# Kernel tuning notes

Measured on AMD Instinct MI355X. Metric: run time of the kernel, lower is better.

## Reference

```python
import jax, jax.numpy as jnp
import numpy as np

EPS = 1e-5

def layer_norm(x, g, b):
    mu = jnp.mean(x, axis=-1, keepdims=True)
    var = jnp.mean(jnp.square(x - mu), axis=-1, keepdims=True)
    return (x - mu) * jax.lax.rsqrt(var + EPS) * g + b

def setup_inputs() -> dict:
    key = jax.random.key(0)
    B, N, IN_D, S, D = 64, 4096, 256, 8, 256
    ks = jax.random.split(key, 20)
    scale = lambda fan_in: 1.0 / np.sqrt(fan_in)
    u = lambda k, shape, s: jax.random.uniform(k, shape, jnp.float32, -s, s)
    return {
        "inputs": jax.random.normal(ks[0], (B, N, IN_D), jnp.float32),
        "noise": jax.random.normal(ks[1], (B, S, D), jnp.float32),
        "slots_mu": jax.random.normal(ks[2], (1, S, D), jnp.float32),
        "slots_sigma": jnp.ones((1, S, D), jnp.float32) * 0.1,
        "Wq": u(ks[3], (D, D), scale(D)), "bq": u(ks[4], (D,), scale(D)),
        "Wk": u(ks[5], (D, IN_D), scale(IN_D)), "bk": u(ks[6], (D,), scale(IN_D)),
        "Wv": u(ks[7], (D, IN_D), scale(IN_D)), "bv": u(ks[8], (D,), scale(IN_D)),
        "W_ih": u(ks[9], (3 * D, D), scale(D)), "b_ih": u(ks[10], (3 * D,), scale(D)),
        "W_hh": u(ks[11], (3 * D, D), scale(D)), "b_hh": u(ks[12], (3 * D,), scale(D)),
        "W1": u(ks[13], (D, D), scale(D)), "b1": u(ks[14], (D,), scale(D)),
        "W2": u(ks[15], (D, D), scale(D)), "b2": u(ks[16], (D,), scale(D)),
        "ln_slots_g": jnp.ones((D,), jnp.float32), "ln_slots_b": jnp.zeros((D,), jnp.float32),
        "ln_mlp_g": jnp.ones((D,), jnp.float32), "ln_mlp_b": jnp.zeros((D,), jnp.float32),
    }

def gru_cell(x, h, W_ih, b_ih, W_hh, b_hh):
    # PyTorch GRUCell: gates ordered (reset, update, new)
    gi = x @ W_ih.T + b_ih  # [B*S, 3D]
    gh = h @ W_hh.T + b_hh
    i_r, i_z, i_n = jnp.split(gi, 3, axis=-1)
    h_r, h_z, h_n = jnp.split(gh, 3, axis=-1)
    r = jax.nn.sigmoid(i_r + h_r)
    z = jax.nn.sigmoid(i_z + h_z)
    n = jnp.tanh(i_n + r * h_n)
    return (1.0 - z) * n + z * h

def reference(inputs, noise, slots_mu, slots_sigma, Wq, bq, Wk, bk, Wv, bv,
              W_ih, b_ih, W_hh, b_hh, W1, b1, W2, b2,
              ln_slots_g, ln_slots_b, ln_mlp_g, ln_mlp_b):
    B, N, _ = inputs.shape
    _, S, D = noise.shape
    num_iterations = 3
    slots = slots_mu + slots_sigma * noise  # [B, S, D]
    # k, v are loop-invariant; hoist the big GEMMs out of the iteration loop
    k = jnp.einsum('bnd,ed->bne', inputs, Wk) + bk  # [B, N, D]
    v = jnp.einsum('bnd,ed->bne', inputs, Wv) + bv  # [B, N, D]
    inv_sqrt_d = 1.0 / np.sqrt(D)
    for _ in range(num_iterations):
        slots_prev = slots
        q = layer_norm(slots, ln_slots_g, ln_slots_b) @ Wq.T + bq  # [B, S, D]
        attn_logits = jnp.einsum('bsd,bnd->bsn', q, k) * inv_sqrt_d
        attn = jax.nn.softmax(attn_logits, axis=-1)  # softmax over inputs (dim=-1)
        updates = jnp.einsum('bsn,bnd->bsd', attn, v)  # [B, S, D]
        h_new = gru_cell(updates.reshape(-1, D), slots_prev.reshape(-1, D),
                         W_ih, b_ih, W_hh, b_hh).reshape(B, S, D)
        slots = slots_prev + h_new  # residual around GRU (as in source)
        hidden = jax.nn.relu(layer_norm(slots, ln_mlp_g, ln_mlp_b) @ W1.T + b1)
        slots = slots + (hidden @ W2.T + b2)
    return slots
```

## Files before the change

kernel.cpp:

```cpp
#include <hip/hip_runtime.h>


constexpr int Bn = 64;
constexpr int Nn = 4096;
constexpr int Dd = 256;
constexpr int Ss = 8;
constexpr int CH = 16;
constexpr float EPSF = 1e-5f;

#define DEV __device__ __forceinline__

using short8 = __attribute__((ext_vector_type(8))) short;
using f32x4 = __attribute__((ext_vector_type(4))) float;
union U8 { short8 s; uint4 u; };

DEV unsigned bfpack2(float lo, float hi) {
  unsigned ul = __float_as_uint(lo), uh = __float_as_uint(hi);
  ul = (ul + 0x7FFFu + ((ul >> 16) & 1u)) >> 16;
  uh = (uh + 0x7FFFu + ((uh >> 16) & 1u)) & 0xFFFF0000u;
  return ul | uh;
}
DEV unsigned short bf16r(float x) {
  unsigned u = __float_as_uint(x);
  u = (u + 0x7FFFu + ((u >> 16) & 1u)) >> 16;
  return (unsigned short)u;
}
DEV float rsum32(float v) {
  v += __shfl_xor(v, 1); v += __shfl_xor(v, 2); v += __shfl_xor(v, 4);
  v += __shfl_xor(v, 8); v += __shfl_xor(v, 16);
  return v;
}
DEV float sigm(float x) { return 1.f / (1.f + __expf(-x)); }

template <int NK>
DEV void load_af(short8* a, const unsigned short* base, int lda, int m16, int quad) {
  const unsigned short* p = base + m16 * lda + quad * 8;
#pragma unroll
  for (int kk = 0; kk < NK; ++kk) a[kk] = *(const short8*)(p + kk * 32);
}
template <int NK>
DEV f32x4 gemm_tile(const short8* a, const unsigned short* wr, float binit) {
  f32x4 acc = {binit, binit, binit, binit};
#pragma unroll
  for (int kk = 0; kk < NK; ++kk) {
    short8 b = *(const short8*)(wr + kk * 32);
    acc = __builtin_amdgcn_mfma_f32_16x16x32_bf16(a[kk], b, acc, 0, 0, 0);
  }
  return acc;
}

DEV void ln_row8(const float* x, const float* g, const float* b, int d0,
                 unsigned short* dst) {
  float s = x[0] + x[1] + x[2] + x[3] + x[4] + x[5] + x[6] + x[7];
  float mu = rsum32(s) * (1.f / 256.f);
  float q = 0.f;
#pragma unroll
  for (int j = 0; j < 8; ++j) { float d = x[j] - mu; q += d * d; }
  float rs = rsqrtf(rsum32(q) * (1.f / 256.f) + EPSF);
  float o[8];
#pragma unroll
  for (int j = 0; j < 8; ++j) o[j] = (x[j] - mu) * rs * g[d0 + j] + b[d0 + j];
  uint4 w;
  w.x = bfpack2(o[0], o[1]); w.y = bfpack2(o[2], o[3]);
  w.z = bfpack2(o[4], o[5]); w.w = bfpack2(o[6], o[7]);
  *(uint4*)dst = w;
}

__global__ __launch_bounds__(256) void k_wqk(const float* __restrict__ Wq,
                                             const float* __restrict__ Wk,
                                             const float* __restrict__ bq,
                                             unsigned short* __restrict__ Wqk_b,
                                             float* __restrict__ bqk) {
  int tid = threadIdx.x, c = blockIdx.x;
  if (c < 256) {
    float acc = 0.f;
    for (int e = 0; e < 256; ++e) acc += Wq[e * 256 + tid] * Wk[e * 256 + c];
    Wqk_b[c * 256 + tid] = bf16r(acc);
  } else {
    float acc = 0.f;
    for (int e = 0; e < 256; ++e) acc += bq[e] * Wk[e * 256 + tid];
    bqk[tid] = acc;
  }
}

__global__ __launch_bounds__(256) void k_conv(
    const float* __restrict__ Wv, const float* __restrict__ Wih,
    const float* __restrict__ Whh, const float* __restrict__ W1,
    const float* __restrict__ W2,
    const float* __restrict__ bih, const float* __restrict__ bhh,
    unsigned* Wv_b, unsigned* Wzr_b, unsigned* Win_b, unsigned* Whn_b,
    unsigned* W1_b, unsigned* W2_b, float* bzr) {
  if (blockIdx.x >= 1152) {
    int i = (blockIdx.x - 1152) * 256 + threadIdx.x;
    if (i < 512) bzr[i] = bih[i] + bhh[i];
    return;
  }
  int p = blockIdx.x * 256 + threadIdx.x;
  const float* src; unsigned* dst;
  if (p < 32768) { src = Wv + 2 * p; dst = Wv_b + p; }
  else if (p < 163840) {
    int q = p - 32768, row = q >> 8, col = (q & 255) * 2;
    src = (col < 256) ? (Wih + row * 256 + col) : (Whh + row * 256 + col - 256);
    dst = Wzr_b + q;
  }
  else if (p < 196608) { int q = p - 163840; src = Wih + 512 * 256 + 2 * q; dst = Win_b + q; }
  else if (p < 229376) { int q = p - 196608; src = Whh + 512 * 256 + 2 * q; dst = Whn_b + q; }
  else if (p < 262144) { int q = p - 229376; src = W1 + 2 * q; dst = W1_b + q; }
  else { int q = p - 262144; src = W2 + 2 * q; dst = W2_b + q; }
  dst[0] = bfpack2(src[0], src[1]);
}

__global__ __launch_bounds__(512) void k_qk0(const float* __restrict__ noise,
                                             const float* __restrict__ s_mu,
                                             const float* __restrict__ s_sg,
                                             const float* __restrict__ gsl,
                                             const float* __restrict__ bsl,
                                             const unsigned short* __restrict__ Wqk_b,
                                             const float* __restrict__ bqk,
                                             float* __restrict__ slots,
                                             float* __restrict__ qk) {
  __shared__ __align__(16) unsigned short lnb[16 * 264];
  const int tid = threadIdx.x, bb = blockIdx.x;
  const int lane = tid & 63, wave = tid >> 6;
  const int m16 = lane & 15, quad = lane >> 4;
  const int row = tid >> 5, l32 = tid & 31, d0 = l32 * 8;
  {
    const int grow = bb * 16 + row;
    const int sidx = (grow & 7) * 256 + d0;
    const float* np = noise + (size_t)grow * 256 + d0;
    float4 n0 = *(const float4*)np, n1 = *(const float4*)(np + 4);
    float4 m0 = *(const float4*)(s_mu + sidx), m1 = *(const float4*)(s_mu + sidx + 4);
    float4 g0 = *(const float4*)(s_sg + sidx), g1 = *(const float4*)(s_sg + sidx + 4);
    float x[8] = {m0.x + g0.x * n0.x, m0.y + g0.y * n0.y,
                  m0.z + g0.z * n0.z, m0.w + g0.w * n0.w,
                  m1.x + g1.x * n1.x, m1.y + g1.y * n1.y,
                  m1.z + g1.z * n1.z, m1.w + g1.w * n1.w};
    float* sp_ = slots + (size_t)grow * 256 + d0;
    float4 o0, o1;
    o0.x = x[0]; o0.y = x[1]; o0.z = x[2]; o0.w = x[3];
    o1.x = x[4]; o1.y = x[5]; o1.z = x[6]; o1.w = x[7];
    *(float4*)sp_ = o0; *(float4*)(sp_ + 4) = o1;
    ln_row8(x, gsl, bsl, d0, lnb + row * 264 + d0);
  }
  __syncthreads();
  short8 a8[8];
  load_af<8>(a8, lnb, 264, m16, quad);
#pragma unroll
  for (int i = 0; i < 2; ++i) {
    int t = wave + 8 * i;
    f32x4 acc = gemm_tile<8>(a8, Wqk_b + (size_t)(t * 16 + m16) * 256 + quad * 8,
                             bqk[t * 16 + m16]);
#pragma unroll
    for (int r = 0; r < 4; ++r)
      qk[(size_t)(bb * 16 + quad * 4 + r) * 256 + t * 16 + m16] = acc[r] * 0.0625f;
  }
}

template <bool FIRST>
DEV void ld_chunk(const float* __restrict__ xin, unsigned* __restrict__ xbf,
                  size_t nbase, int tid, uint4* pr) {
#pragma unroll
  for (int i = 0; i < 8; ++i) {
    int flat = i * 256 + tid, n = flat >> 5, od = flat & 31;
    if (FIRST) {
      const float4* src = (const float4*)(xin + (nbase + n) * 256 + od * 8);
      float4 v0 = src[0], v1 = src[1];
      uint4 o;
      o.x = bfpack2(v0.x, v0.y); o.y = bfpack2(v0.z, v0.w);
      o.z = bfpack2(v1.x, v1.y); o.w = bfpack2(v1.z, v1.w);
      ((uint4*)xbf)[(nbase + n) * 32 + od] = o;
      pr[i] = o;
    } else {
      pr[i] = ((const uint4*)xbf)[(nbase + n) * 32 + od];
    }
  }
}

template <bool FIRST>
__global__ __launch_bounds__(256) void k_attn(const float* __restrict__ xin,
                                              unsigned* __restrict__ xbf,
                                              const float* __restrict__ qk,
                                              float* __restrict__ pl,
                                              float* __restrict__ pu) {
  __shared__ __align__(16) unsigned xt[128 * 65];
  __shared__ __align__(16) unsigned pp[32 * 17];
  __shared__ __align__(16) float lred[4][16];
  const int tid = threadIdx.x;
  const int lane = tid & 63, wave = tid >> 6;
  const int m16 = lane & 15, quad = lane >> 4;
  const int c = blockIdx.x, b = blockIdx.y;
  const int pb = (b * CH + c) * 8;
  const unsigned psel = (m16 & 1) ? 0x07060302u : 0x05040100u;

  short8 aq[8];
  {
    const float* qrow = qk + (size_t)(b * 8 + (m16 & 7)) * 256 + quad * 8;
#pragma unroll
    for (int kk = 0; kk < 8; ++kk) {
      U8 f;
      float4 q0 = *(const float4*)(qrow + kk * 32);
      float4 q1 = *(const float4*)(qrow + kk * 32 + 4);
      f.u.x = bfpack2(q0.x, q0.y); f.u.y = bfpack2(q0.z, q0.w);
      f.u.z = bfpack2(q1.x, q1.y); f.u.w = bfpack2(q1.z, q1.w);
      if (m16 >= 8) { f.u.x = 0u; f.u.y = 0u; f.u.z = 0u; f.u.w = 0u; }
      aq[kk] = f.s;
    }
  }
  float lacc[4] = {0.f, 0.f, 0.f, 0.f};
  f32x4 acc[4];
#pragma unroll
  for (int t = 0; t < 4; ++t) acc[t] = (f32x4){0.f, 0.f, 0.f, 0.f};
  const int d0w = wave * 64;

  uint4 pr[8];
  const size_t nb0 = (size_t)b * Nn + (size_t)c * 256;
  ld_chunk<FIRST>(xin, xbf, nb0, tid, pr);

  for (int ch = 0; ch < 4; ++ch) {
#pragma unroll
    for (int i = 0; i < 8; ++i) {
      int flat = i * 256 + tid, n = flat >> 5, od = flat & 31, rb = od * 4;
      xt[(rb + 0) * 65 + n] = pr[i].x;
      xt[(rb + 1) * 65 + n] = pr[i].y;
      xt[(rb + 2) * 65 + n] = pr[i].z;
      xt[(rb + 3) * 65 + n] = pr[i].w;
    }
    __syncthreads();
    if (ch + 1 < 4)
      ld_chunk<FIRST>(xin, xbf, nb0 + (size_t)(ch + 1) * 64, tid, pr);
    {
      const int nt = wave;
      f32x4 pacc = (f32x4){0.f, 0.f, 0.f, 0.f};
#pragma unroll
      for (int kk = 0; kk < 8; ++kk) {
        int base = (kk * 16 + quad * 4) * 65 + nt * 16 + m16;
        U8 bf;
        bf.u.x = xt[base]; bf.u.y = xt[base + 65];
        bf.u.z = xt[base + 130]; bf.u.w = xt[base + 195];
        pacc = __builtin_amdgcn_mfma_f32_16x16x32_bf16(aq[kk], bf.s, pacc, 0, 0, 0);
      }
      const int xrow = nt * 16 + m16;
      unsigned short* pps = (unsigned short*)pp;
#pragma unroll
      for (int r = 0; r < 4; ++r) {
        float p = __expf(pacc[r]);
        lacc[r] += p;
        pps[((xrow >> 1) * 17 + quad * 4 + r) * 2 + (xrow & 1)] = bf16r(p);
      }
    }
    __syncthreads();
#pragma unroll
    for (int nh = 0; nh < 2; ++nh) {
      U8 bp;
      bp.u.x = pp[(nh * 16 + quad * 4 + 0) * 17 + m16];
      bp.u.y = pp[(nh * 16 + quad * 4 + 1) * 17 + m16];
      bp.u.z = pp[(nh * 16 + quad * 4 + 2) * 17 + m16];
      bp.u.w = pp[(nh * 16 + quad * 4 + 3) * 17 + m16];
#pragma unroll
      for (int t = 0; t < 4; ++t) {
        int d = d0w + t * 16 + m16;
        const unsigned* xr = xt + (d >> 1) * 65 + nh * 32 + quad * 8;
        unsigned u0 = xr[0], u1 = xr[1], u2 = xr[2], u3 = xr[3];
        unsigned u4 = xr[4], u5 = xr[5], u6 = xr[6], u7 = xr[7];
        U8 af;
        af.u.x = __builtin_amdgcn_perm(u1, u0, psel);
        af.u.y = __builtin_amdgcn_perm(u3, u2, psel);
        af.u.z = __builtin_amdgcn_perm(u5, u4, psel);
        af.u.w = __builtin_amdgcn_perm(u7, u6, psel);
        acc[t] = __builtin_amdgcn_mfma_f32_16x16x32_bf16(af.s, bp.s, acc[t], 0, 0, 0);
      }
    }
    __syncthreads();
  }
  if (m16 < 8) {
#pragma unroll
    for (int t = 0; t < 4; ++t)
#pragma unroll
      for (int r = 0; r < 4; ++r)
        pu[(size_t)(pb + m16) * 256 + d0w + t * 16 + quad * 4 + r] = acc[t][r];
  }
  {
#pragma unroll
    for (int r = 0; r < 4; ++r) {
      float v = lacc[r];
      v += __shfl_xor(v, 1); v += __shfl_xor(v, 2);
      v += __shfl_xor(v, 4); v += __shfl_xor(v, 8);
      if (m16 == 0) lred[wave][quad * 4 + r] = v;
    }
  }
  __syncthreads();
  if (tid < 8)
    pl[pb + tid] = lred[0][tid] + lred[1][tid] + lred[2][tid] + lred[3][tid];
}

__global__ __launch_bounds__(512) void k_upd(
    const float* __restrict__ pl, const float* __restrict__ pu,
    const unsigned short* __restrict__ Wv_b, const float* __restrict__ bv,
    const unsigned short* __restrict__ Wzr_b, const float* __restrict__ bzr,
    const unsigned short* __restrict__ Win_b, const float* __restrict__ bin,
    const unsigned short* __restrict__ Whn_b, const float* __restrict__ bhn,
    const unsigned short* __restrict__ W1_b, const float* __restrict__ b1,
    const unsigned short* __restrict__ W2_b, const float* __restrict__ b2,
    const float* __restrict__ gml, const float* __restrict__ bml,
    const float* __restrict__ gsl, const float* __restrict__ bsl,
    const unsigned short* __restrict__ Wqk_b, const float* __restrict__ bqk,
    float* __restrict__ slots, float* __restrict__ qk, float* __restrict__ dout) {
  __shared__ __align__(16) unsigned short cat[16 * 520];
  __shared__ __align__(16) float sp[16 * 260];
  __shared__ __align__(16) float s1[16 * 260];
  __shared__ __align__(16) unsigned short lnb[16 * 264];
  const int tid = threadIdx.x, bb = blockIdx.x;
  const int lane = tid & 63, wave = tid >> 6;
  const int m16 = lane & 15, quad = lane >> 4;
  const int row = tid >> 5, l32 = tid & 31, d0 = l32 * 8;
  const int bat = 2 * bb + (row >> 3), sl = row & 7;
  {
    float L = 0.f;
#pragma unroll
    for (int cc = 0; cc < 16; ++cc) L += pl[(bat * 16 + cc) * 8 + sl];
    float li = 1.f / L;
    float a[8] = {0.f, 0.f, 0.f, 0.f, 0.f, 0.f, 0.f, 0.f};
    for (int cc = 0; cc < 16; ++cc) {
      const float* pp_ = pu + ((size_t)(bat * 16 + cc) * 8 + sl) * 256 + d0;
      float4 v0 = *(const float4*)pp_, v1 = *(const float4*)(pp_ + 4);
      a[0] += v0.x; a[1] += v0.y; a[2] += v0.z; a[3] += v0.w;
      a[4] += v1.x; a[5] += v1.y; a[6] += v1.z; a[7] += v1.w;
    }
    uint4 o;
    o.x = bfpack2(a[0] * li, a[1] * li); o.y = bfpack2(a[2] * li, a[3] * li);
    o.z = bfpack2(a[4] * li, a[5] * li); o.w = bfpack2(a[6] * li, a[7] * li);
    *(uint4*)(cat + row * 520 + d0) = o;
    const float* sp_ = slots + (size_t)(bb * 16 + row) * 256 + d0;
    float4 h0 = *(const float4*)sp_, h1 = *(const float4*)(sp_ + 4);
    *(float4*)(sp + row * 260 + d0) = h0;
    *(float4*)(sp + row * 260 + d0 + 4) = h1;
    uint4 hb;
    hb.x = bfpack2(h0.x, h0.y); hb.y = bfpack2(h0.z, h0.w);
    hb.z = bfpack2(h1.x, h1.y); hb.w = bfpack2(h1.z, h1.w);
    *(uint4*)(cat + row * 520 + 256 + d0) = hb;
  }
  __syncthreads();
  short8 afr[16];
  load_af<8>(afr, cat, 520, m16, quad);
  f32x4 accv[2];
#pragma unroll
// ... 89 lines not shown
    f32x4 acc = gemm_tile<8>(afr, Wqk_b + (size_t)(t * 16 + m16) * 256 + quad * 8,
                             bqk[t * 16 + m16]);
#pragma unroll
    for (int r = 0; r < 4; ++r)
      qk[(size_t)(bb * 16 + quad * 4 + r) * 256 + t * 16 + m16] = acc[r] * 0.0625f;
  }
}

extern "C" void kernel_launch(void* const* d_in, const int* in_sizes, int n_in,
                              void* d_out, int out_size, void* d_ws, size_t ws_size,
                              hipStream_t stream) {
  const float* inputs = (const float*)d_in[0];
  const float* noise = (const float*)d_in[1];
  const float* s_mu = (const float*)d_in[2];
  const float* s_sg = (const float*)d_in[3];
  const float* Wq = (const float*)d_in[4];
  const float* bq = (const float*)d_in[5];
  const float* Wk = (const float*)d_in[6];
  const float* Wv = (const float*)d_in[8];
  const float* bv = (const float*)d_in[9];
  const float* Wih = (const float*)d_in[10];
  const float* bih = (const float*)d_in[11];
  const float* Whh = (const float*)d_in[12];
  const float* bhh = (const float*)d_in[13];
  const float* W1 = (const float*)d_in[14];
  const float* b1 = (const float*)d_in[15];
  const float* W2 = (const float*)d_in[16];
  const float* b2 = (const float*)d_in[17];
  const float* gsl = (const float*)d_in[18];
  const float* bsl = (const float*)d_in[19];
  const float* gml = (const float*)d_in[20];
  const float* bml = (const float*)d_in[21];
  float* out = (float*)d_out;

  char* wsb = (char*)d_ws;
  unsigned* xbf = (unsigned*)wsb;
  float* fp = (float*)(wsb + (size_t)Bn * Nn * Dd * 2);
  float* slots = fp; fp += Bn * Ss * Dd;
  float* qk = fp;    fp += Bn * Ss * Dd;
  float* bqk = fp;   fp += Dd;
  float* pl = fp;    fp += Bn * CH * Ss;
  float* pu = fp;    fp += Bn * CH * Ss * Dd;
  float* bzr = fp;   fp += 512;
  unsigned short* wb = (unsigned short*)fp;
  unsigned short* Wv_b = wb;  wb += 65536;
  unsigned short* Wzr_b = wb; wb += 262144;
  unsigned short* Win_b = wb; wb += 65536;
  unsigned short* Whn_b = wb; wb += 65536;
  unsigned short* W1_b = wb;  wb += 65536;
  unsigned short* W2_b = wb;  wb += 65536;
  unsigned short* Wqk_b = wb; wb += 65536;
  (void)in_sizes; (void)n_in; (void)out_size; (void)ws_size;

  k_wqk<<<dim3(257), dim3(256), 0, stream>>>(Wq, Wk, bq, Wqk_b, bqk);
  k_conv<<<dim3(1154), dim3(256), 0, stream>>>(
      Wv, Wih, Whh, W1, W2, bih, bhh, (unsigned*)Wv_b, (unsigned*)Wzr_b,
      (unsigned*)Win_b, (unsigned*)Whn_b, (unsigned*)W1_b, (unsigned*)W2_b, bzr);
  k_qk0<<<dim3(32), dim3(512), 0, stream>>>(noise, s_mu, s_sg, gsl, bsl, Wqk_b, bqk,
                                            slots, qk);
  for (int it = 0; it < 3; ++it) {
    if (it == 0)
      k_attn<true><<<dim3(CH, Bn), dim3(256), 0, stream>>>(inputs, xbf, qk, pl, pu);
    else
      k_attn<false><<<dim3(CH, Bn), dim3(256), 0, stream>>>(nullptr, xbf, qk, pl, pu);
    k_upd<<<dim3(32), dim3(512), 0, stream>>>(
        pl, pu, Wv_b, bv, Wzr_b, bzr, Win_b, bih + 512, Whn_b, bhh + 512, W1_b, b1,
        W2_b, b2, gml, bml, gsl, bsl, Wqk_b, bqk, slots, qk, (it == 2) ? out : nullptr);
  }
}
```

Baseline: 686.5 us.

## Fuse whole pipeline into one cooperative persistent kernel with grid syncs

Replaces the sequence of nine kernel launches (weight prep, qk0, three attention/update pairs) with a single cooperative kernel of 1024 blocks that separates stages with grid.sync and reuses shared memory through a union. The update stage is rewritten for 256-thread blocks so it fits the shared launch shape. The aim is to remove launch gaps and per-kernel tail effects. In exchange only 32 of the 1024 blocks do work during the update and qk0 phases, grid-wide barriers add cost, and the launch falls back to the old path if the cooperative launch fails (for example when 1024 blocks cannot all be resident).

```diff
diff --git a/kernel.cpp b/kernel.cpp
--- a/kernel.cpp
+++ b/kernel.cpp
@@ -1,4 +1,7 @@
 #include <hip/hip_runtime.h>
+#include <hip/hip_cooperative_groups.h>
+
+namespace cg = cooperative_groups;
 
 
 constexpr int Bn = 64;
@@ -64,6 +67,413 @@
   w.x = bfpack2(o[0], o[1]); w.y = bfpack2(o[2], o[3]);
   w.z = bfpack2(o[4], o[5]); w.w = bfpack2(o[6], o[7]);
   *(uint4*)dst = w;
+}
+
+
+template <bool FIRST>
+DEV void ld_chunk_t(const float* __restrict__ xin, unsigned* __restrict__ xbf,
+                    size_t nbase, int tid, uint4* pr) {
+#pragma unroll
+  for (int i = 0; i < 8; ++i) {
+    int flat = i * 256 + tid, n = flat >> 5, od = flat & 31;
+    if (FIRST) {
+      const float4* src = (const float4*)(xin + (nbase + n) * 256 + od * 8);
+      float4 v0 = src[0], v1 = src[1];
+      uint4 o;
+      o.x = bfpack2(v0.x, v0.y); o.y = bfpack2(v0.z, v0.w);
+      o.z = bfpack2(v1.x, v1.y); o.w = bfpack2(v1.z, v1.w);
+      ((uint4*)xbf)[(nbase + n) * 32 + od] = o;
+      pr[i] = o;
+    } else {
+      pr[i] = ((const uint4*)xbf)[(nbase + n) * 32 + od];
+    }
+  }
+}
+DEV void ld_chunk_rt(bool first, const float* __restrict__ xin,
+                     unsigned* __restrict__ xbf, size_t nbase, int tid, uint4* pr) {
+  if (first) ld_chunk_t<true>(xin, xbf, nbase, tid, pr);
+  else ld_chunk_t<false>(xin, xbf, nbase, tid, pr);
+}
+
+DEV void attn_unit(const float* __restrict__ xin, unsigned* __restrict__ xbf,
+                   const float* __restrict__ qk, float* __restrict__ pl,
+                   float* __restrict__ pu, unsigned* xt, unsigned* pp,
+                   float (*lred)[16], int u, bool first, int tid) {
+  const int lane = tid & 63, wave = tid >> 6;
+  const int m16 = lane & 15, quad = lane >> 4;
+  const int b = u >> 4, c = u & 15;
+  const int pb = u * 8;
+  const unsigned psel = (m16 & 1) ? 0x07060302u : 0x05040100u;
+
+  short8 aq[8];
+  {
+    const float* qrow = qk + (size_t)(b * 8 + (m16 & 7)) * 256 + quad * 8;
+#pragma unroll
+    for (int kk = 0; kk < 8; ++kk) {
+      U8 f;
+      float4 q0 = *(const float4*)(qrow + kk * 32);
+      float4 q1 = *(const float4*)(qrow + kk * 32 + 4);
+      f.u.x = bfpack2(q0.x, q0.y); f.u.y = bfpack2(q0.z, q0.w);
+      f.u.z = bfpack2(q1.x, q1.y); f.u.w = bfpack2(q1.z, q1.w);
+      if (m16 >= 8) { f.u.x = 0u; f.u.y = 0u; f.u.z = 0u; f.u.w = 0u; }
+      aq[kk] = f.s;
+    }
+  }
+  float lacc[4] = {0.f, 0.f, 0.f, 0.f};
+  f32x4 acc[4];
+#pragma unroll
+  for (int t = 0; t < 4; ++t) acc[t] = (f32x4){0.f, 0.f, 0.f, 0.f};
+  const int d0w = wave * 64;
+
+  uint4 pr[8];
+  const size_t nb0 = (size_t)b * Nn + (size_t)c * 256;
+  ld_chunk_rt(first, xin, xbf, nb0, tid, pr);
+
+  for (int ch = 0; ch < 4; ++ch) {
+#pragma unroll
+    for (int i = 0; i < 8; ++i) {
+      int flat = i * 256 + tid, n = flat >> 5, od = flat & 31, rb = od * 4;
+      xt[(rb + 0) * 65 + n] = pr[i].x;
+      xt[(rb + 1) * 65 + n] = pr[i].y;
+      xt[(rb + 2) * 65 + n] = pr[i].z;
+      xt[(rb + 3) * 65 + n] = pr[i].w;
+    }
+    __syncthreads();
+    if (ch + 1 < 4)
+      ld_chunk_rt(first, xin, xbf, nb0 + (size_t)(ch + 1) * 64, tid, pr);
+    {
+      const int nt = wave;
+      f32x4 pacc = (f32x4){0.f, 0.f, 0.f, 0.f};
+#pragma unroll
+      for (int kk = 0; kk < 8; ++kk) {
+        int base = (kk * 16 + quad * 4) * 65 + nt * 16 + m16;
+        U8 bf;
+        bf.u.x = xt[base]; bf.u.y = xt[base + 65];
+        bf.u.z = xt[base + 130]; bf.u.w = xt[base + 195];
+        pacc = __builtin_amdgcn_mfma_f32_16x16x32_bf16(aq[kk], bf.s, pacc, 0, 0, 0);
+      }
+      const int xrow = nt * 16 + m16;
+      unsigned short* pps = (unsigned short*)pp;
+#pragma unroll
+      for (int r = 0; r < 4; ++r) {
+        float p = __expf(pacc[r]);
+        lacc[r] += p;
+        pps[((xrow >> 1) * 17 + quad * 4 + r) * 2 + (xrow & 1)] = bf16r(p);
+      }
+    }
+    __syncthreads();
+#pragma unroll
+    for (int nh = 0; nh < 2; ++nh) {
+      U8 bp;
+      bp.u.x = pp[(nh * 16 + quad * 4 + 0) * 17 + m16];
+      bp.u.y = pp[(nh * 16 + quad * 4 + 1) * 17 + m16];
+      bp.u.z = pp[(nh * 16 + quad * 4 + 2) * 17 + m16];
+      bp.u.w = pp[(nh * 16 + quad * 4 + 3) * 17 + m16];
+#pragma unroll
+      for (int t = 0; t < 4; ++t) {
+        int d = d0w + t * 16 + m16;
+        const unsigned* xr = xt + (d >> 1) * 65 + nh * 32 + quad * 8;
+        unsigned u0 = xr[0], u1 = xr[1], u2 = xr[2], u3 = xr[3];
+        unsigned u4 = xr[4], u5 = xr[5], u6 = xr[6], u7 = xr[7];
+        U8 af;
+        af.u.x = __builtin_amdgcn_perm(u1, u0, psel);
+        af.u.y = __builtin_amdgcn_perm(u3, u2, psel);
+        af.u.z = __builtin_amdgcn_perm(u5, u4, psel);
+        af.u.w = __builtin_amdgcn_perm(u7, u6, psel);
+        acc[t] = __builtin_amdgcn_mfma_f32_16x16x32_bf16(af.s, bp.s, acc[t], 0, 0, 0);
+      }
+    }
+    __syncthreads();
+  }
+  if (m16 < 8) {
+#pragma unroll
+    for (int t = 0; t < 4; ++t)
+#pragma unroll
+      for (int r = 0; r < 4; ++r)
+        pu[(size_t)(pb + m16) * 256 + d0w + t * 16 + quad * 4 + r] = acc[t][r];
+  }
+#pragma unroll
+  for (int r = 0; r < 4; ++r) {
+    float v = lacc[r];
+    v += __shfl_xor(v, 1); v += __shfl_xor(v, 2);
+    v += __shfl_xor(v, 4); v += __shfl_xor(v, 8);
+    if (m16 == 0) lred[wave][quad * 4 + r] = v;
+  }
+  __syncthreads();
+  if (tid < 8)
+    pl[pb + tid] = lred[0][tid] + lred[1][tid] + lred[2][tid] + lred[3][tid];
+}
+
+DEV void upd_body256(
+    const float* __restrict__ pl, const float* __restrict__ pu,
+    const unsigned short* __restrict__ Wv_b, const float* __restrict__ bv,
+    const unsigned short* __restrict__ Wzr_b, const float* __restrict__ bzr,
+    const unsigned short* __restrict__ Win_b, const float* __restrict__ bin,
+    const unsigned short* __restrict__ Whn_b, const float* __restrict__ bhn,
+    const unsigned short* __restrict__ W1_b, const float* __restrict__ b1,
+    const unsigned short* __restrict__ W2_b, const float* __restrict__ b2,
+    const float* __restrict__ gml, const float* __restrict__ bml,
+    const float* __restrict__ gsl, const float* __restrict__ bsl,
+    const unsigned short* __restrict__ Wqk_b, const float* __restrict__ bqk,
+    float* __restrict__ slots, float* __restrict__ qk, float* __restrict__ dout,
+    unsigned short* cat, float* sp, int bb, int tid) {
+  unsigned short* lnbp = cat + 256;
+  const int lane = tid & 63, wave4 = tid >> 6;
+  const int m16 = lane & 15, quad = lane >> 4;
+  const int row8 = tid >> 5, l32 = tid & 31, d0 = l32 * 8;
+#pragma unroll
+  for (int r2 = 0; r2 < 2; ++r2) {
+    const int row = row8 + 8 * r2;
+    const int bat = 2 * bb + (row >> 3), sl = row & 7;
+    float L = 0.f;
+#pragma unroll
+    for (int cc = 0; cc < 16; ++cc) L += pl[(bat * 16 + cc) * 8 + sl];
+    float li = 1.f / L;
+    float a[8] = {0.f, 0.f, 0.f, 0.f, 0.f, 0.f, 0.f, 0.f};
+    for (int cc = 0; cc < 16; ++cc) {
+      const float* pp_ = pu + ((size_t)(bat * 16 + cc) * 8 + sl) * 256 + d0;
+      float4 v0 = *(const float4*)pp_, v1 = *(const float4*)(pp_ + 4);
+      a[0] += v0.x; a[1] += v0.y; a[2] += v0.z; a[3] += v0.w;
+      a[4] += v1.x; a[5] += v1.y; a[6] += v1.z; a[7] += v1.w;
+    }
+    uint4 o;
+    o.x = bfpack2(a[0] * li, a[1] * li); o.y = bfpack2(a[2] * li, a[3] * li);
+    o.z = bfpack2(a[4] * li, a[5] * li); o.w = bfpack2(a[6] * li, a[7] * li);
+    *(uint4*)(cat + row * 520 + d0) = o;
+    const float* sp_ = slots + (size_t)(bb * 16 + row) * 256 + d0;
+    float4 h0 = *(const float4*)sp_, h1 = *(const float4*)(sp_ + 4);
+    *(float4*)(sp + row * 260 + d0) = h0;
+    *(float4*)(sp + row * 260 + d0 + 4) = h1;
+    uint4 hb;
+    hb.x = bfpack2(h0.x, h0.y); hb.y = bfpack2(h0.z, h0.w);
+    hb.z = bfpack2(h1.x, h1.y); hb.w = bfpack2(h1.z, h1.w);
+    *(uint4*)(cat + row * 520 + 256 + d0) = hb;
+  }
+  __syncthreads();
+  short8 afr[16];
+  load_af<8>(afr, cat, 520, m16, quad);
+  f32x4 accv[4];
+#pragma unroll
+  for (int i = 0; i < 4; ++i) {
+    int t = wave4 + 4 * i;
+    accv[i] = gemm_tile<8>(afr, Wv_b + (size_t)(t * 16 + m16) * 256 + quad * 8,
+                           bv[t * 16 + m16]);
+  }
+  __syncthreads();
+#pragma unroll
+  for (int i = 0; i < 4; ++i) {
+    int t = wave4 + 4 * i;
+#pragma unroll
+    for (int r = 0; r < 4; ++r)
+      cat[(quad * 4 + r) * 520 + t * 16 + m16] = bf16r(accv[i][r]);
+  }
+  __syncthreads();
+  load_af<16>(afr, cat, 520, m16, quad);
+#pragma unroll
+  for (int i = 0; i < 4; ++i) {
+    int t = wave4 + 4 * i, col = t * 16 + m16;
+    f32x4 ar = gemm_tile<16>(afr, Wzr_b + (size_t)(t * 16 + m16) * 512 + quad * 8,
+                             bzr[t * 16 + m16]);
+    f32x4 az = gemm_tile<16>(afr, Wzr_b + (size_t)((t + 16) * 16 + m16) * 512 + quad * 8,
+                             bzr[(t + 16) * 16 + m16]);
+    f32x4 ain = gemm_tile<8>(afr, Win_b + (size_t)(t * 16 + m16) * 256 + quad * 8,
+                             bin[col]);
+    f32x4 ahn = gemm_tile<8>(afr + 8, Whn_b + (size_t)(t * 16 + m16) * 256 + quad * 8,
+                             bhn[col]);
+#pragma unroll
+    for (int r = 0; r < 4; ++r) {
+      int rw = quad * 4 + r;
+      float rrv = sigm(ar[r]), zzv = sigm(az[r]);
+      float nin = ain[r] + rrv * ahn[r];
+      float nn = 1.f - 2.f / (__expf(2.f * nin) + 1.f);
+      float hpc = sp[rw * 260 + col];
+      sp[rw * 260 + col] = hpc + (1.f - zzv) * nn + zzv * hpc;
+    }
+  }
+  __syncthreads();
+#pragma unroll
+  for (int r2 = 0; r2 < 2; ++r2) {
+    int row = row8 + 8 * r2;
+    const float* s1r = sp + row * 260 + d0;
+    float4 v0 = *(const float4*)s1r, v1 = *(const float4*)(s1r + 4);
+    float x[8] = {v0.x, v0.y, v0.z, v0.w, v1.x, v1.y, v1.z, v1.w};
+    ln_row8(x, gml, bml, d0, lnbp + row * 520 + d0);
+  }
+  __syncthreads();
+  load_af<8>(afr, lnbp, 520, m16, quad);
+#pragma unroll
+  for (int i = 0; i < 4; ++i) {
+    int t = wave4 + 4 * i;
+    f32x4 acc = gemm_tile<8>(afr, W1_b + (size_t)(t * 16 + m16) * 256 + quad * 8,
+                             b1[t * 16 + m16]);
+#pragma unroll
+    for (int r = 0; r < 4; ++r)
+      cat[(quad * 4 + r) * 520 + t * 16 + m16] = bf16r(fmaxf(acc[r], 0.f));
+  }
+  __syncthreads();
+  load_af<8>(afr, cat, 520, m16, quad);
+#pragma unroll
+  for (int i = 0; i < 4; ++i) {
+    int t = wave4 + 4 * i;
+    f32x4 acc = gemm_tile<8>(afr, W2_b + (size_t)(t * 16 + m16) * 256 + quad * 8,
+                             b2[t * 16 + m16]);
+#pragma unroll
+    for (int r = 0; r < 4; ++r) {
+      int rw = quad * 4 + r, col = t * 16 + m16;
+      float v = acc[r] + sp[rw * 260 + col];
+      size_t gi = (size_t)(bb * 16 + rw) * 256 + col;
+      slots[gi] = v;
+      if (dout) dout[gi] = v;
+      sp[rw * 260 + col] = v;
+    }
+  }
+  __syncthreads();
+#pragma unroll
+  for (int r2 = 0; r2 < 2; ++r2) {
+    int row = row8 + 8 * r2;
+    const float* spr = sp + row * 260 + d0;
+    float4 v0 = *(const float4*)spr, v1 = *(const float4*)(spr + 4);
+    float x[8] = {v0.x, v0.y, v0.z, v0.w, v1.x, v1.y, v1.z, v1.w};
+    ln_row8(x, gsl, bsl, d0, lnbp + row * 520 + d0);
+  }
+  __syncthreads();
+  load_af<8>(afr, lnbp, 520, m16, quad);
+#pragma unroll
+  for (int i = 0; i < 4; ++i) {
+    int t = wave4 + 4 * i;
+    f32x4 acc = gemm_tile<8>(afr, Wqk_b + (size_t)(t * 16 + m16) * 256 + quad * 8,
+                             bqk[t * 16 + m16]);
+#pragma unroll
+    for (int r = 0; r < 4; ++r)
+      qk[(size_t)(bb * 16 + quad * 4 + r) * 256 + t * 16 + m16] = acc[r] * 0.0625f;
+  }
+}
+
+DEV void qk0_body256(const float* __restrict__ noise, const float* __restrict__ s_mu,
+                     const float* __restrict__ s_sg, const float* __restrict__ gsl,
+                     const float* __restrict__ bsl,
+                     const unsigned short* __restrict__ Wqk_b,
+                     const float* __restrict__ bqk, float* __restrict__ slots,
+                     float* __restrict__ qk, unsigned short* cat, int bb, int tid) {
+  unsigned short* lnbp = cat + 256;
+  const int lane = tid & 63, wave4 = tid >> 6;
+  const int m16 = lane & 15, quad = lane >> 4;
+  const int row8 = tid >> 5, l32 = tid & 31, d0 = l32 * 8;
+#pragma unroll
+  for (int r2 = 0; r2 < 2; ++r2) {
+    const int row = row8 + 8 * r2;
+    const int grow = bb * 16 + row;
+    const int sidx = (grow & 7) * 256 + d0;
+    const float* np = noise + (size_t)grow * 256 + d0;
+    float4 n0 = *(const float4*)np, n1 = *(const float4*)(np + 4);
+    float4 m0 = *(const float4*)(s_mu + sidx), m1 = *(const float4*)(s_mu + sidx + 4);
+    float4 g0 = *(const float4*)(s_sg + sidx), g1 = *(const float4*)(s_sg + sidx + 4);
+    float x[8] = {m0.x + g0.x * n0.x, m0.y + g0.y * n0.y,
+                  m0.z + g0.z * n0.z, m0.w + g0.w * n0.w,
+                  m1.x + g1.x * n1.x, m1.y + g1.y * n1.y,
+                  m1.z + g1.z * n1.z, m1.w + g1.w * n1.w};
+    float* sp_ = slots + (size_t)grow * 256 + d0;
+    float4 o0, o1;
+    o0.x = x[0]; o0.y = x[1]; o0.z = x[2]; o0.w = x[3];
+    o1.x = x[4]; o1.y = x[5]; o1.z = x[6]; o1.w = x[7];
+    *(float4*)sp_ = o0; *(float4*)(sp_ + 4) = o1;
+    ln_row8(x, gsl, bsl, d0, lnbp + row * 520 + d0);
+  }
+  __syncthreads();
+  short8 a8[8];
+  load_af<8>(a8, lnbp, 520, m16, quad);
+#pragma unroll
+  for (int i = 0; i < 4; ++i) {
+    int t = wave4 + 4 * i;
+    f32x4 acc = gemm_tile<8>(a8, Wqk_b + (size_t)(t * 16 + m16) * 256 + quad * 8,
+                             bqk[t * 16 + m16]);
+#pragma unroll
+    for (int r = 0; r < 4; ++r)
+      qk[(size_t)(bb * 16 + quad * 4 + r) * 256 + t * 16 + m16] = acc[r] * 0.0625f;
+  }
+}
+
+DEV void prep_unit(int u, int tid,
+                   const float* Wq, const float* Wk, const float* bq,
+                   unsigned short* Wqk_b, float* bqk,
+                   const float* Wv, const float* Wih, const float* Whh,
+                   const float* W1, const float* W2,
+                   const float* bih, const float* bhh,
+                   unsigned* Wv_b, unsigned* Wzr_b, unsigned* Win_b, unsigned* Whn_b,
+                   unsigned* W1_b, unsigned* W2_b, float* bzr) {
+  if (u < 256) {
+    float acc = 0.f;
+    for (int e = 0; e < 256; ++e) acc += Wq[e * 256 + tid] * Wk[e * 256 + u];
+    Wqk_b[u * 256 + tid] = bf16r(acc);
+  } else if (u == 256) {
+    float acc = 0.f;
+    for (int e = 0; e < 256; ++e) acc += bq[e] * Wk[e * 256 + tid];
+    bqk[tid] = acc;
+  } else {
+    int cu = u - 257;
+    if (cu >= 1152) {
+      int i = (cu - 1152) * 256 + tid;
+      if (i < 512) bzr[i] = bih[i] + bhh[i];
+      return;
+    }
+    int p = cu * 256 + tid;
+    const float* src; unsigned* dst;
+    if (p < 32768) { src = Wv + 2 * p; dst = Wv_b + p; }
+    else if (p < 163840) {
+      int q = p - 32768, row = q >> 8, col = (q & 255) * 2;
+      src = (col < 256) ? (Wih + row * 256 + col) : (Whh + row * 256 + col - 256);
+      dst = Wzr_b + q;
+    }
+    else if (p < 196608) { int q = p - 163840; src = Wih + 512 * 256 + 2 * q; dst = Win_b + q; }
+    else if (p < 229376) { int q = p - 196608; src = Whh + 512 * 256 + 2 * q; dst = Whn_b + q; }
+    else if (p < 262144) { int q = p - 229376; src = W1 + 2 * q; dst = W1_b + q; }
+    else { int q = p - 262144; src = W2 + 2 * q; dst = W2_b + q; }
+    dst[0] = bfpack2(src[0], src[1]);
+  }
+}
+
+struct MegaArgs {
+  const float *inputs, *noise, *s_mu, *s_sg;
+  const float *Wq, *bq, *Wk, *Wv, *bv, *Wih, *bih, *Whh, *bhh;
+  const float *W1, *b1, *W2, *b2, *gsl, *bsl, *gml, *bml;
+  unsigned* xbf;
+  float *slots, *qk, *bqk, *pl, *pu, *bzr;
+  unsigned short *Wv_b, *Wzr_b, *Win_b, *Whn_b, *W1_b, *W2_b, *Wqk_b;
+  float* out;
+};
+
+__global__ __launch_bounds__(256, 4) void k_mega(MegaArgs a) {
+  __shared__ __align__(16) union SMU {
+    struct { unsigned xt[128 * 65]; unsigned pp[32 * 17]; float lred[4][16]; } at;
+    struct { unsigned short cat[16 * 520]; float sp[16 * 260]; } up;
+  } sm;
+  const int tid = threadIdx.x, bid = blockIdx.x;
+  cg::grid_group grid = cg::this_grid();
+  for (int u = bid; u < 1411; u += (int)gridDim.x)
+    prep_unit(u, tid, a.Wq, a.Wk, a.bq, a.Wqk_b, a.bqk, a.Wv, a.Wih, a.Whh, a.W1,
+              a.W2, a.bih, a.bhh, (unsigned*)a.Wv_b, (unsigned*)a.Wzr_b,
+              (unsigned*)a.Win_b, (unsigned*)a.Whn_b, (unsigned*)a.W1_b,
+              (unsigned*)a.W2_b, a.bzr);
+  __threadfence();
+  grid.sync();
+  if (bid < 32)
+    qk0_body256(a.noise, a.s_mu, a.s_sg, a.gsl, a.bsl, a.Wqk_b, a.bqk, a.slots, a.qk,
+                sm.up.cat, bid, tid);
+  __threadfence();
+  grid.sync();
+  for (int it = 0; it < 3; ++it) {
+    attn_unit(a.inputs, a.xbf, a.qk, a.pl, a.pu, sm.at.xt, sm.at.pp, sm.at.lred,
+              bid, it == 0, tid);
+    __threadfence();
+    grid.sync();
+    if (bid < 32)
+      upd_body256(a.pl, a.pu, a.Wv_b, a.bv, a.Wzr_b, a.bzr, a.Win_b, a.bih + 512,
+                  a.Whn_b, a.bhh + 512, a.W1_b, a.b1, a.W2_b, a.b2, a.gml, a.bml,
+                  a.gsl, a.bsl, a.Wqk_b, a.bqk, a.slots, a.qk,
+                  (it == 2) ? a.out : nullptr, sm.up.cat, sm.up.sp, bid, tid);
+    __threadfence();
+    grid.sync();
+  }
 }
 
 __global__ __launch_bounds__(256) void k_wqk(const float* __restrict__ Wq,
@@ -157,26 +567,6 @@
 }
 
 template <bool FIRST>
-DEV void ld_chunk(const float* __restrict__ xin, unsigned* __restrict__ xbf,
-                  size_t nbase, int tid, uint4* pr) {
-#pragma unroll
-  for (int i = 0; i < 8; ++i) {
-    int flat = i * 256 + tid, n = flat >> 5, od = flat & 31;
-    if (FIRST) {
-      const float4* src = (const float4*)(xin + (nbase + n) * 256 + od * 8);
-      float4 v0 = src[0], v1 = src[1];
-      uint4 o;
-      o.x = bfpack2(v0.x, v0.y); o.y = bfpack2(v0.z, v0.w);
-      o.z = bfpack2(v1.x, v1.y); o.w = bfpack2(v1.z, v1.w);
-      ((uint4*)xbf)[(nbase + n) * 32 + od] = o;
-      pr[i] = o;
-    } else {
-      pr[i] = ((const uint4*)xbf)[(nbase + n) * 32 + od];
-    }
-  }
-}
-
-template <bool FIRST>
 __global__ __launch_bounds__(256) void k_attn(const float* __restrict__ xin,
                                               unsigned* __restrict__ xbf,
                                               const float* __restrict__ qk,
@@ -185,112 +575,8 @@
   __shared__ __align__(16) unsigned xt[128 * 65];
   __shared__ __align__(16) unsigned pp[32 * 17];
   __shared__ __align__(16) float lred[4][16];
-  const int tid = threadIdx.x;
-  const int lane = tid & 63, wave = tid >> 6;
-  const int m16 = lane & 15, quad = lane >> 4;
-  const int c = blockIdx.x, b = blockIdx.y;
-  const int pb = (b * CH + c) * 8;
-  const unsigned psel = (m16 & 1) ? 0x07060302u : 0x05040100u;
-
-  short8 aq[8];
-  {
-    const float* qrow = qk + (size_t)(b * 8 + (m16 & 7)) * 256 + quad * 8;
-#pragma unroll
-    for (int kk = 0; kk < 8; ++kk) {
-      U8 f;
-      float4 q0 = *(const float4*)(qrow + kk * 32);
-      float4 q1 = *(const float4*)(qrow + kk * 32 + 4);
-      f.u.x = bfpack2(q0.x, q0.y); f.u.y = bfpack2(q0.z, q0.w);
-      f.u.z = bfpack2(q1.x, q1.y); f.u.w = bfpack2(q1.z, q1.w);
-      if (m16 >= 8) { f.u.x = 0u; f.u.y = 0u; f.u.z = 0u; f.u.w = 0u; }
-      aq[kk] = f.s;
-    }
-  }
-  float lacc[4] = {0.f, 0.f, 0.f, 0.f};
-  f32x4 acc[4];
-#pragma unroll
-  for (int t = 0; t < 4; ++t) acc[t] = (f32x4){0.f, 0.f, 0.f, 0.f};
-  const int d0w = wave * 64;
-
-  uint4 pr[8];
-  const size_t nb0 = (size_t)b * Nn + (size_t)c * 256;
-  ld_chunk<FIRST>(xin, xbf, nb0, tid, pr);
-
-  for (int ch = 0; ch < 4; ++ch) {
-#pragma unroll
-    for (int i = 0; i < 8; ++i) {
-      int flat = i * 256 + tid, n = flat >> 5, od = flat & 31, rb = od * 4;
-      xt[(rb + 0) * 65 + n] = pr[i].x;
-      xt[(rb + 1) * 65 + n] = pr[i].y;
-      xt[(rb + 2) * 65 + n] = pr[i].z;
-      xt[(rb + 3) * 65 + n] = pr[i].w;
-    }
-    __syncthreads();
-    if (ch + 1 < 4)
-      ld_chunk<FIRST>(xin, xbf, nb0 + (size_t)(ch + 1) * 64, tid, pr);
-    {
-      const int nt = wave;
-      f32x4 pacc = (f32x4){0.f, 0.f, 0.f, 0.f};
-#pragma unroll
-      for (int kk = 0; kk < 8; ++kk) {
-        int base = (kk * 16 + quad * 4) * 65 + nt * 16 + m16;
-        U8 bf;
-        bf.u.x = xt[base]; bf.u.y = xt[base + 65];
-        bf.u.z = xt[base + 130]; bf.u.w = xt[base + 195];
-        pacc = __builtin_amdgcn_mfma_f32_16x16x32_bf16(aq[kk], bf.s, pacc, 0, 0, 0);
-      }
-      const int xrow = nt * 16 + m16;
-      unsigned short* pps = (unsigned short*)pp;
-#pragma unroll
-      for (int r = 0; r < 4; ++r) {
-        float p = __expf(pacc[r]);
-        lacc[r] += p;
-        pps[((xrow >> 1) * 17 + quad * 4 + r) * 2 + (xrow & 1)] = bf16r(p);
-      }
-    }
-    __syncthreads();
-#pragma unroll
-    for (int nh = 0; nh < 2; ++nh) {
-      U8 bp;
-      bp.u.x = pp[(nh * 16 + quad * 4 + 0) * 17 + m16];
-      bp.u.y = pp[(nh * 16 + quad * 4 + 1) * 17 + m16];
-      bp.u.z = pp[(nh * 16 + quad * 4 + 2) * 17 + m16];
-      bp.u.w = pp[(nh * 16 + quad * 4 + 3) * 17 + m16];
-#pragma unroll
-      for (int t = 0; t < 4; ++t) {
-        int d = d0w + t * 16 + m16;
-        const unsigned* xr = xt + (d >> 1) * 65 + nh * 32 + quad * 8;
-        unsigned u0 = xr[0], u1 = xr[1], u2 = xr[2], u3 = xr[3];
-        unsigned u4 = xr[4], u5 = xr[5], u6 = xr[6], u7 = xr[7];
-        U8 af;
-        af.u.x = __builtin_amdgcn_perm(u1, u0, psel);
-        af.u.y = __builtin_amdgcn_perm(u3, u2, psel);
-        af.u.z = __builtin_amdgcn_perm(u5, u4, psel);
-        af.u.w = __builtin_amdgcn_perm(u7, u6, psel);
-        acc[t] = __builtin_amdgcn_mfma_f32_16x16x32_bf16(af.s, bp.s, acc[t], 0, 0, 0);
-      }
-    }
-    __syncthreads();
-  }
-  if (m16 < 8) {
-#pragma unroll
-    for (int t = 0; t < 4; ++t)
-#pragma unroll
-      for (int r = 0; r < 4; ++r)
-        pu[(size_t)(pb + m16) * 256 + d0w + t * 16 + quad * 4 + r] = acc[t][r];
-  }
-  {
-#pragma unroll
-    for (int r = 0; r < 4; ++r) {
-      float v = lacc[r];
-      v += __shfl_xor(v, 1); v += __shfl_xor(v, 2);
-      v += __shfl_xor(v, 4); v += __shfl_xor(v, 8);
-      if (m16 == 0) lred[wave][quad * 4 + r] = v;
-    }
-  }
-  __syncthreads();
-  if (tid < 8)
-    pl[pb + tid] = lred[0][tid] + lred[1][tid] + lred[2][tid] + lred[3][tid];
+  const int u = (int)blockIdx.y * CH + (int)blockIdx.x;
+  attn_unit(xin, xbf, qk, pl, pu, xt, pp, lred, u, FIRST, threadIdx.x);
 }
 
 __global__ __launch_bounds__(512) void k_upd(
@@ -486,19 +772,36 @@
   unsigned short* Wqk_b = wb; wb += 65536;
   (void)in_sizes; (void)n_in; (void)out_size; (void)ws_size;
 
-  k_wqk<<<dim3(257), dim3(256), 0, stream>>>(Wq, Wk, bq, Wqk_b, bqk);
-  k_conv<<<dim3(1154), dim3(256), 0, stream>>>(
-      Wv, Wih, Whh, W1, W2, bih, bhh, (unsigned*)Wv_b, (unsigned*)Wzr_b,
-      (unsigned*)Win_b, (unsigned*)Whn_b, (unsigned*)W1_b, (unsigned*)W2_b, bzr);
-  k_qk0<<<dim3(32), dim3(512), 0, stream>>>(noise, s_mu, s_sg, gsl, bsl, Wqk_b, bqk,
-                                            slots, qk);
-  for (int it = 0; it < 3; ++it) {
-    if (it == 0)
-      k_attn<true><<<dim3(CH, Bn), dim3(256), 0, stream>>>(inputs, xbf, qk, pl, pu);
-    else
-      k_attn<false><<<dim3(CH, Bn), dim3(256), 0, stream>>>(nullptr, xbf, qk, pl, pu);
-    k_upd<<<dim3(32), dim3(512), 0, stream>>>(
-        pl, pu, Wv_b, bv, Wzr_b, bzr, Win_b, bih + 512, Whn_b, bhh + 512, W1_b, b1,
-        W2_b, b2, gml, bml, gsl, bsl, Wqk_b, bqk, slots, qk, (it == 2) ? out : nullptr);
-  }
-}
+  MegaArgs ma;
+  ma.inputs = inputs; ma.noise = noise; ma.s_mu = s_mu; ma.s_sg = s_sg;
+  ma.Wq = Wq; ma.bq = bq; ma.Wk = Wk; ma.Wv = Wv; ma.bv = bv;
+  ma.Wih = Wih; ma.bih = bih; ma.Whh = Whh; ma.bhh = bhh;
+  ma.W1 = W1; ma.b1 = b1; ma.W2 = W2; ma.b2 = b2;
+  ma.gsl = gsl; ma.bsl = bsl; ma.gml = gml; ma.bml = bml;
+  ma.xbf = xbf; ma.slots = slots; ma.qk = qk; ma.bqk = bqk;
+  ma.pl = pl; ma.pu = pu; ma.bzr = bzr;
+  ma.Wv_b = Wv_b; ma.Wzr_b = Wzr_b; ma.Win_b = Win_b; ma.Whn_b = Whn_b;
+  ma.W1_b = W1_b; ma.W2_b = W2_b; ma.Wqk_b = Wqk_b;
+  ma.out = out;
+  void* kargs[] = {(void*)&ma};
+  hipError_t err = hipLaunchCooperativeKernel((const void*)k_mega, dim3(1024),
+                                              dim3(256), kargs, 0, stream);
+  if (err != hipSuccess) {
+    (void)hipGetLastError();
+    k_wqk<<<dim3(257), dim3(256), 0, stream>>>(Wq, Wk, bq, Wqk_b, bqk);
+    k_conv<<<dim3(1154), dim3(256), 0, stream>>>(
+        Wv, Wih, Whh, W1, W2, bih, bhh, (unsigned*)Wv_b, (unsigned*)Wzr_b,
+        (unsigned*)Win_b, (unsigned*)Whn_b, (unsigned*)W1_b, (unsigned*)W2_b, bzr);
+    k_qk0<<<dim3(32), dim3(512), 0, stream>>>(noise, s_mu, s_sg, gsl, bsl, Wqk_b, bqk,
+                                              slots, qk);
+    for (int it = 0; it < 3; ++it) {
+      if (it == 0)
+        k_attn<true><<<dim3(CH, Bn), dim3(256), 0, stream>>>(inputs, xbf, qk, pl, pu);
+      else
+        k_attn<false><<<dim3(CH, Bn), dim3(256), 0, stream>>>(nullptr, xbf, qk, pl, pu);
+      k_upd<<<dim3(32), dim3(512), 0, stream>>>(
+          pl, pu, Wv_b, bv, Wzr_b, bzr, Win_b, bih + 512, Whn_b, bhh + 512, W1_b, b1,
+          W2_b, b2, gml, bml, gsl, bsl, Wqk_b, bqk, slots, qk, (it == 2) ? out : nullptr);
+    }
+  }
+}
```

Measured after the change: 2.592 ms. 3.78x slower.

## Split input bf16 conversion into separate kernel and double-buffer attention LDS

Applied to the files above, without the earlier changes.

Moves the fp32-to-bf16 conversion of the inputs out of the first attention pass into a standalone streaming kernel, so one attention kernel serves all iterations. The attention kernel double-buffers its transposed-x and probability LDS tiles, which removes the trailing barrier per chunk. The logits MFMA now takes its B operand straight from global memory instead of the LDS transpose. The intent is to cut barrier stalls and LDS bank traffic. In exchange it doubles LDS use, which may lower occupancy, and adds redundant global reads of x.

```diff
diff --git a/kernel.cpp b/kernel.cpp
--- a/kernel.cpp
+++ b/kernel.cpp
@@ -108,6 +108,20 @@
   else if (p < 262144) { int q = p - 229376; src = W1 + 2 * q; dst = W1_b + q; }
   else { int q = p - 262144; src = W2 + 2 * q; dst = W2_b + q; }
   dst[0] = bfpack2(src[0], src[1]);
+}
+
+__global__ __launch_bounds__(256) void k_xconv(const float* __restrict__ xin,
+                                               unsigned* __restrict__ xbf) {
+#pragma unroll
+  for (int j = 0; j < 4; ++j) {
+    int flat = blockIdx.x * 1024 + j * 256 + threadIdx.x;
+    const float4* src = (const float4*)(xin + (size_t)flat * 8);
+    float4 v0 = src[0], v1 = src[1];
+    uint4 o;
+    o.x = bfpack2(v0.x, v0.y); o.y = bfpack2(v0.z, v0.w);
+    o.z = bfpack2(v1.x, v1.y); o.w = bfpack2(v1.z, v1.w);
+    ((uint4*)xbf)[flat] = o;
+  }
 }
 
 __global__ __launch_bounds__(512) void k_qk0(const float* __restrict__ noise,
@@ -156,34 +170,12 @@
   }
 }
 
-template <bool FIRST>
-DEV void ld_chunk(const float* __restrict__ xin, unsigned* __restrict__ xbf,
-                  size_t nbase, int tid, uint4* pr) {
-#pragma unroll
-  for (int i = 0; i < 8; ++i) {
-    int flat = i * 256 + tid, n = flat >> 5, od = flat & 31;
-    if (FIRST) {
-      const float4* src = (const float4*)(xin + (nbase + n) * 256 + od * 8);
-      float4 v0 = src[0], v1 = src[1];
-      uint4 o;
-      o.x = bfpack2(v0.x, v0.y); o.y = bfpack2(v0.z, v0.w);
-      o.z = bfpack2(v1.x, v1.y); o.w = bfpack2(v1.z, v1.w);
-      ((uint4*)xbf)[(nbase + n) * 32 + od] = o;
-      pr[i] = o;
-    } else {
-      pr[i] = ((const uint4*)xbf)[(nbase + n) * 32 + od];
-    }
-  }
-}
-
-template <bool FIRST>
-__global__ __launch_bounds__(256) void k_attn(const float* __restrict__ xin,
-                                              unsigned* __restrict__ xbf,
+__global__ __launch_bounds__(256) void k_attn(const unsigned* __restrict__ xbf,
                                               const float* __restrict__ qk,
                                               float* __restrict__ pl,
                                               float* __restrict__ pu) {
-  __shared__ __align__(16) unsigned xt[128 * 65];
-  __shared__ __align__(16) unsigned pp[32 * 17];
+  __shared__ __align__(16) unsigned xt[2][128 * 65];
+  __shared__ __align__(16) unsigned pp[2][32 * 17];
   __shared__ __align__(16) float lred[4][16];
   const int tid = threadIdx.x;
   const int lane = tid & 63, wave = tid >> 6;
@@ -212,54 +204,67 @@
   for (int t = 0; t < 4; ++t) acc[t] = (f32x4){0.f, 0.f, 0.f, 0.f};
   const int d0w = wave * 64;
 
+  const size_t row0 = (size_t)b * Nn + (size_t)c * 256;
+  const uint4* xb4 = (const uint4*)xbf;
+
   uint4 pr[8];
-  const size_t nb0 = (size_t)b * Nn + (size_t)c * 256;
-  ld_chunk<FIRST>(xin, xbf, nb0, tid, pr);
+#pragma unroll
+  for (int i = 0; i < 8; ++i) {
+    int flat = i * 256 + tid, n = flat >> 5, od = flat & 31;
+    pr[i] = xb4[(row0 + n) * 32 + od];
+  }
 
   for (int ch = 0; ch < 4; ++ch) {
+    const int p = ch & 1;
+    unsigned* xtb = xt[p];
 #pragma unroll
     for (int i = 0; i < 8; ++i) {
       int flat = i * 256 + tid, n = flat >> 5, od = flat & 31, rb = od * 4;
-      xt[(rb + 0) * 65 + n] = pr[i].x;
-      xt[(rb + 1) * 65 + n] = pr[i].y;
-      xt[(rb + 2) * 65 + n] = pr[i].z;
-      xt[(rb + 3) * 65 + n] = pr[i].w;
-    }
-    __syncthreads();
-    if (ch + 1 < 4)
-      ld_chunk<FIRST>(xin, xbf, nb0 + (size_t)(ch + 1) * 64, tid, pr);
+      xtb[(rb + 0) * 65 + n] = pr[i].x;
+      xtb[(rb + 1) * 65 + n] = pr[i].y;
+      xtb[(rb + 2) * 65 + n] = pr[i].z;
+      xtb[(rb + 3) * 65 + n] = pr[i].w;
+    }
+    if (ch + 1 < 4) {
+      const size_t nb = row0 + (size_t)(ch + 1) * 64;
+#pragma unroll
+      for (int i = 0; i < 8; ++i) {
+        int flat = i * 256 + tid, n = flat >> 5, od = flat & 31;
+        pr[i] = xb4[(nb + n) * 32 + od];
+      }
+    }
     {
       const int nt = wave;
+      const size_t arow = row0 + (size_t)ch * 64 + nt * 16 + m16;
       f32x4 pacc = (f32x4){0.f, 0.f, 0.f, 0.f};
 #pragma unroll
       for (int kk = 0; kk < 8; ++kk) {
-        int base = (kk * 16 + quad * 4) * 65 + nt * 16 + m16;
         U8 bf;
-        bf.u.x = xt[base]; bf.u.y = xt[base + 65];
-        bf.u.z = xt[base + 130]; bf.u.w = xt[base + 195];
+        bf.u = xb4[arow * 32 + kk * 4 + quad];
         pacc = __builtin_amdgcn_mfma_f32_16x16x32_bf16(aq[kk], bf.s, pacc, 0, 0, 0);
       }
       const int xrow = nt * 16 + m16;
-      unsigned short* pps = (unsigned short*)pp;
+      unsigned short* pps = (unsigned short*)pp[p];
 #pragma unroll
       for (int r = 0; r < 4; ++r) {
-        float p = __expf(pacc[r]);
-        lacc[r] += p;
-        pps[((xrow >> 1) * 17 + quad * 4 + r) * 2 + (xrow & 1)] = bf16r(p);
+        float pv = __expf(pacc[r]);
+        lacc[r] += pv;
+        pps[((xrow >> 1) * 17 + quad * 4 + r) * 2 + (xrow & 1)] = bf16r(pv);
       }
     }
     __syncthreads();
+    const unsigned* ppb = pp[p];
 #pragma unroll
     for (int nh = 0; nh < 2; ++nh) {
       U8 bp;
-      bp.u.x = pp[(nh * 16 + quad * 4 + 0) * 17 + m16];
-      bp.u.y = pp[(nh * 16 + quad * 4 + 1) * 17 + m16];
-      bp.u.z = pp[(nh * 16 + quad * 4 + 2) * 17 + m16];
-      bp.u.w = pp[(nh * 16 + quad * 4 + 3) * 17 + m16];
+      bp.u.x = ppb[(nh * 16 + quad * 4 + 0) * 17 + m16];
+      bp.u.y = ppb[(nh * 16 + quad * 4 + 1) * 17 + m16];
+      bp.u.z = ppb[(nh * 16 + quad * 4 + 2) * 17 + m16];
+      bp.u.w = ppb[(nh * 16 + quad * 4 + 3) * 17 + m16];
 #pragma unroll
       for (int t = 0; t < 4; ++t) {
         int d = d0w + t * 16 + m16;
-        const unsigned* xr = xt + (d >> 1) * 65 + nh * 32 + quad * 8;
+        const unsigned* xr = xtb + (d >> 1) * 65 + nh * 32 + quad * 8;
         unsigned u0 = xr[0], u1 = xr[1], u2 = xr[2], u3 = xr[3];
         unsigned u4 = xr[4], u5 = xr[5], u6 = xr[6], u7 = xr[7];
         U8 af;
@@ -270,7 +275,6 @@
         acc[t] = __builtin_amdgcn_mfma_f32_16x16x32_bf16(af.s, bp.s, acc[t], 0, 0, 0);
       }
     }
-    __syncthreads();
   }
   if (m16 < 8) {
 #pragma unroll
@@ -279,14 +283,12 @@
       for (int r = 0; r < 4; ++r)
         pu[(size_t)(pb + m16) * 256 + d0w + t * 16 + quad * 4 + r] = acc[t][r];
   }
-  {
-#pragma unroll
-    for (int r = 0; r < 4; ++r) {
-      float v = lacc[r];
-      v += __shfl_xor(v, 1); v += __shfl_xor(v, 2);
-      v += __shfl_xor(v, 4); v += __shfl_xor(v, 8);
-      if (m16 == 0) lred[wave][quad * 4 + r] = v;
-    }
+#pragma unroll
+  for (int r = 0; r < 4; ++r) {
+    float v = lacc[r];
+    v += __shfl_xor(v, 1); v += __shfl_xor(v, 2);
+    v += __shfl_xor(v, 4); v += __shfl_xor(v, 8);
+    if (m16 == 0) lred[wave][quad * 4 + r] = v;
   }
   __syncthreads();
   if (tid < 8)
@@ -486,6 +488,7 @@
   unsigned short* Wqk_b = wb; wb += 65536;
   (void)in_sizes; (void)n_in; (void)out_size; (void)ws_size;
 
+  k_xconv<<<dim3(8192), dim3(256), 0, stream>>>(inputs, xbf);
   k_wqk<<<dim3(257), dim3(256), 0, stream>>>(Wq, Wk, bq, Wqk_b, bqk);
   k_conv<<<dim3(1154), dim3(256), 0, stream>>>(
       Wv, Wih, Whh, W1, W2, bih, bhh, (unsigned*)Wv_b, (unsigned*)Wzr_b,
@@ -493,10 +496,7 @@
   k_qk0<<<dim3(32), dim3(512), 0, stream>>>(noise, s_mu, s_sg, gsl, bsl, Wqk_b, bqk,
                                             slots, qk);
   for (int it = 0; it < 3; ++it) {
-    if (it == 0)
-      k_attn<true><<<dim3(CH, Bn), dim3(256), 0, stream>>>(inputs, xbf, qk, pl, pu);
-    else
-      k_attn<false><<<dim3(CH, Bn), dim3(256), 0, stream>>>(nullptr, xbf, qk, pl, pu);
+    k_attn<<<dim3(CH, Bn), dim3(256), 0, stream>>>(xbf, qk, pl, pu);
     k_upd<<<dim3(32), dim3(512), 0, stream>>>(
         pl, pu, Wv_b, bv, Wzr_b, bzr, Win_b, bih + 512, Whn_b, bhh + 512, W1_b, b1,
         W2_b, b2, gml, bml, gsl, bsl, Wqk_b, bqk, slots, qk, (it == 2) ? out : nullptr);
```

Measured after the change: 699.1 us. Within noise of the previous version (+1.8%).
